# Kernel tuning notes

Measured on AMD Instinct MI355X. Metric: run time of the kernel, lower is better.

## Reference

```python
import jax, jax.numpy as jnp
import numpy as np

N = 10000      # nodes (docstring: dense mode intended for <=10k nodes)
D_IN = 64      # in_dim
D_OUT = 64     # out_dim


def setup_inputs() -> dict:
    key = jax.random.key(0)
    kH, kA1, kA2, kA3, kW1, kW2, kW3 = jax.random.split(key, 7)
    H = jax.random.normal(kH, (N, D_IN), dtype=jnp.float32)
    # Dense normalized adjacency per edge type (values in [0,1), as in A_norm)
    A_r1 = jax.random.uniform(kA1, (N, N), dtype=jnp.float32)
    A_r2 = jax.random.uniform(kA2, (N, N), dtype=jnp.float32)
    A_r3 = jax.random.uniform(kA3, (N, N), dtype=jnp.float32)
    # Xavier-uniform init for type-specific linear weights [out_dim, in_dim]
    limit = float(np.sqrt(6.0 / (D_IN + D_OUT)))
    W1 = jax.random.uniform(kW1, (D_OUT, D_IN), dtype=jnp.float32, minval=-limit, maxval=limit)
    W2 = jax.random.uniform(kW2, (D_OUT, D_IN), dtype=jnp.float32, minval=-limit, maxval=limit)
    W3 = jax.random.uniform(kW3, (D_OUT, D_IN), dtype=jnp.float32, minval=-limit, maxval=limit)
    bias = jnp.zeros((D_OUT,), dtype=jnp.float32)
    return {"H": H, "A_r1": A_r1, "A_r2": A_r2, "A_r3": A_r3,
            "W1": W1, "W2": W2, "W3": W3, "bias": bias}


def reference(H, A_r1, A_r2, A_r3, W1, W2, W3, bias):
    # h_v = sum_r W_r @ (sum_u A_r[v,u] * h_u) + b  (no activation in forward)
    out = bias  # broadcasts to [N, D_OUT]
    for A_r, W_r in ((A_r1, W1), (A_r2, W2), (A_r3, W3)):
        msg = A_r @ H                      # [N, D_IN] neighbor aggregation
        out = out + msg @ W_r.T            # [N, D_OUT] type-specific projection
    return out
```

## Files before the change

### kernel.cpp

```cpp
#include <hip/hip_runtime.h>

static constexpr int NN = 10000;
static constexpr int DD = 64;
static constexpr int KP = 10240;
static constexpr int BK = 128;
static constexpr int SPLITS = 4;
static constexpr int KC = KP / SPLITS;
static constexpr int ITERS = KC / BK;
static constexpr int BM = 64;

typedef __attribute__((ext_vector_type(4))) float f32x4;
typedef __attribute__((ext_vector_type(8))) short s16x8;

__device__ __forceinline__ unsigned short f2bf(float f) {
  unsigned u = __float_as_uint(f);
  return (unsigned short)((u + 0x7fffu + ((u >> 16) & 1u)) >> 16);
}

__device__ __forceinline__ void g2l16(const void* g, void* l) {
  __builtin_amdgcn_global_load_lds((const __attribute__((address_space(1))) unsigned int*)g,
                                   (__attribute__((address_space(3))) unsigned int*)l, 16, 0, 0);
}

__global__ void prep_kernel(const float* __restrict__ H,
                            const float* __restrict__ W1,
                            const float* __restrict__ W2,
                            const float* __restrict__ W3,
                            unsigned short* __restrict__ mt) {
  const int r = blockIdx.y;
  const float* W = (r == 0) ? W1 : (r == 1) ? W2 : W3;
  const int wave = threadIdx.x >> 6;
  const int lane = threadIdx.x & 63;
  f32x4 wr[16];
#pragma unroll
  for (int i = 0; i < 16; ++i) wr[i] = *(const f32x4*)&W[lane * 64 + i * 4];
  unsigned short* orow = mt + ((size_t)r * 64 + lane) * KP;
  const int kbase = blockIdx.x * 128 + wave * 32;
  for (int i = 0; i < 32; ++i) {
    const int k = kbase + i;
    if (k < NN) {
      float s = 0.f;
#pragma unroll
      for (int j = 0; j < 16; ++j) {
        f32x4 h = *(const f32x4*)&H[(size_t)k * 64 + j * 4];
        s += h[0] * wr[j][0] + h[1] * wr[j][1] + h[2] * wr[j][2] + h[3] * wr[j][3];
      }
      orow[k] = f2bf(s);
    } else {
      orow[k] = 0;
    }
  }
}

__global__ void init_out_kernel(const float* __restrict__ bias, float* __restrict__ out) {
  const int i = blockIdx.x * 256 + threadIdx.x;
  if (i < NN * DD) out[i] = bias[i & 63];
}

__global__ __launch_bounds__(256, 4) void gcn_main(const float* __restrict__ A1,
                                                   const float* __restrict__ A2,
                                                   const float* __restrict__ A3,
                                                   const unsigned short* __restrict__ mt,
                                                   float* __restrict__ out) {
  __shared__ __align__(1024) unsigned short mlds[2][64][128];

  const int r = blockIdx.z;
  const int s = blockIdx.y;
  const float* A = (r == 0) ? A1 : (r == 1) ? A2 : A3;
  const unsigned short* mtr = mt + (size_t)r * 64 * KP;

  const int wave = threadIdx.x >> 6;
  const int lane = threadIdx.x & 63;
  const int l15 = lane & 15;
  const int lhi = lane >> 4;
  const int seg = lane & 15;
  const int r16 = lane >> 4;
  const int v0 = blockIdx.x * BM;
  const int k0 = s * KC;

  int vA = v0 + wave * 16 + l15;
  if (vA > NN - 1) vA = NN - 1;
  const float* arow = A + (size_t)vA * NN;

  f32x4 acc[4] = {{0.f,0.f,0.f,0.f},{0.f,0.f,0.f,0.f},{0.f,0.f,0.f,0.f},{0.f,0.f,0.f,0.f}};
  f32x4 R0[4][2], R1[4][2];

  auto stageM = [&](int t, int buf) {
    const int kb = k0 + t * BK;
#pragma unroll
    for (int j = 0; j < 4; ++j) {
      const int row16 = 4 * j + r16;
      const int rowabs = wave * 16 + row16;
      const unsigned short* src = mtr + (size_t)rowabs * KP + kb + ((seg ^ row16) << 3);
      g2l16(src, &mlds[buf][wave * 16 + 4 * j][0]);
    }
  };

  auto issueA = [&](f32x4 (&a)[4][2], int kb) {
    if (kb + BK <= NN) {
      const float* p = arow + kb + lhi * 8;
      asm volatile(
        "global_load_dwordx4 %0, %8, off\n\t"
        "global_load_dwordx4 %1, %8, off offset:16\n\t"
        "global_load_dwordx4 %2, %8, off offset:128\n\t"
        "global_load_dwordx4 %3, %8, off offset:144\n\t"
        "global_load_dwordx4 %4, %8, off offset:256\n\t"
        "global_load_dwordx4 %5, %8, off offset:272\n\t"
        "global_load_dwordx4 %6, %8, off offset:384\n\t"
        "global_load_dwordx4 %7, %8, off offset:400"
        : "=&v"(a[0][0]), "=&v"(a[0][1]), "=&v"(a[1][0]), "=&v"(a[1][1]),
          "=&v"(a[2][0]), "=&v"(a[2][1]), "=&v"(a[3][0]), "=&v"(a[3][1])
        : "v"(p));
    } else {
      const int kf0 = kb + lhi * 8;
      const float* q0 = arow + ((kf0       < NN) ? kf0       : 0);
      const float* q1 = arow + ((kf0 + 4   < NN) ? kf0 + 4   : 0);
      const float* q2 = arow + ((kf0 + 32  < NN) ? kf0 + 32  : 0);
      const float* q3 = arow + ((kf0 + 36  < NN) ? kf0 + 36  : 0);
      const float* q4 = arow + ((kf0 + 64  < NN) ? kf0 + 64  : 0);
      const float* q5 = arow + ((kf0 + 68  < NN) ? kf0 + 68  : 0);
      const float* q6 = arow + ((kf0 + 96  < NN) ? kf0 + 96  : 0);
      const float* q7 = arow + ((kf0 + 100 < NN) ? kf0 + 100 : 0);
      asm volatile(
        "global_load_dwordx4 %0, %8, off\n\t"
        "global_load_dwordx4 %1, %9, off\n\t"
        "global_load_dwordx4 %2, %10, off\n\t"
        "global_load_dwordx4 %3, %11, off\n\t"
        "global_load_dwordx4 %4, %12, off\n\t"
        "global_load_dwordx4 %5, %13, off\n\t"
        "global_load_dwordx4 %6, %14, off\n\t"
        "global_load_dwordx4 %7, %15, off"
        : "=&v"(a[0][0]), "=&v"(a[0][1]), "=&v"(a[1][0]), "=&v"(a[1][1]),
          "=&v"(a[2][0]), "=&v"(a[2][1]), "=&v"(a[3][0]), "=&v"(a[3][1])
        : "v"(q0), "v"(q1), "v"(q2), "v"(q3), "v"(q4), "v"(q5), "v"(q6), "v"(q7));
    }
  };

  auto cvtA = [&](const f32x4& x, const f32x4& y) -> s16x8 {
    s16x8 v;
    v[0] = (short)f2bf(x[0]); v[1] = (short)f2bf(x[1]);
    v[2] = (short)f2bf(x[2]); v[3] = (short)f2bf(x[3]);
    v[4] = (short)f2bf(y[0]); v[5] = (short)f2bf(y[1]);
    v[6] = (short)f2bf(y[2]); v[7] = (short)f2bf(y[3]);
    return v;
  };

  auto body = [&](int t, f32x4 (&cur)[4][2], f32x4 (&nxt)[4][2]) {
    const int tn = (t + 1 < ITERS) ? t + 1 : ITERS - 1;
    issueA(nxt, k0 + tn * BK);
    stageM(tn, (t + 1) & 1);
    __builtin_amdgcn_sched_barrier(0);
    asm volatile("s_waitcnt vmcnt(12)");
    __builtin_amdgcn_sched_barrier(0);
    __builtin_amdgcn_s_barrier();
    const int kb = k0 + t * BK;
    const int buf = t & 1;
    if (kb + BK > NN) {
      const f32x4 z = {0.f, 0.f, 0.f, 0.f};
#pragma unroll
      for (int kk = 0; kk < 4; ++kk) {
        const int kf = kb + kk * 32 + lhi * 8;
        cur[kk][0] = (kf     >= NN) ? z : cur[kk][0];
        cur[kk][1] = (kf + 4 >= NN) ? z : cur[kk][1];
      }
    }
#pragma unroll
    for (int kk = 0; kk < 4; ++kk) {
      s16x8 a = cvtA(cur[kk][0], cur[kk][1]);
#pragma unroll
      for (int dt = 0; dt < 4; ++dt) {
        const int g = kk * 4 + lhi;
        s16x8 b = *(const s16x8*)&mlds[buf][dt * 16 + l15][((g ^ l15) & 15) * 8];
        acc[dt] = __builtin_amdgcn_mfma_f32_16x16x32_bf16(a, b, acc[dt], 0, 0, 0);
      }
    }
    __builtin_amdgcn_sched_barrier(0);
    __builtin_amdgcn_s_barrier();
  };

  issueA(R0, k0);
  stageM(0, 0);

  for (int t = 0; t < ITERS; t += 2) {
    body(t, R0, R1);
    body(t + 1, R1, R0);
  }

  asm volatile("s_waitcnt vmcnt(0)");

#pragma unroll
  for (int dt = 0; dt < 4; ++dt) {
    const int d = dt * 16 + l15;
#pragma unroll
    for (int i = 0; i < 4; ++i) {
      const int v = v0 + wave * 16 + lhi * 4 + i;
      if (v < NN) atomicAdd(&out[(size_t)v * DD + d], acc[dt][i]);
    }
  }
}

extern "C" void kernel_launch(void* const* d_in, const int* in_sizes, int n_in,
                              void* d_out, int out_size, void* d_ws, size_t ws_size,
                              hipStream_t stream) {
  const float* H    = (const float*)d_in[0];
  const float* A1   = (const float*)d_in[1];
  const float* A2   = (const float*)d_in[2];
  const float* A3   = (const float*)d_in[3];
  const float* W1   = (const float*)d_in[4];
  const float* W2   = (const float*)d_in[5];
  const float* W3   = (const float*)d_in[6];
  const float* bias = (const float*)d_in[7];
  float* out = (float*)d_out;
  unsigned short* mt = (unsigned short*)d_ws;

  prep_kernel<<<dim3(KP / 128, 3), 256, 0, stream>>>(H, W1, W2, W3, mt);
  init_out_kernel<<<dim3((NN * DD + 255) / 256), 256, 0, stream>>>(bias, out);
  gcn_main<<<dim3((NN + BM - 1) / BM, SPLITS, 3), 256, 0, stream>>>(A1, A2, A3, mt, out);
}
```

Baseline: 310.1 us.

## Stage whole M chunk in LDS once and raise K splits

Raises the K split count so each block handles only four 128-wide K tiles. The block's full 64x512 bf16 slice of the projected features is loaded into LDS once up front, replacing per-tile double-buffered staging and the two barriers per iteration. The A loads then run as a fixed, fully unrolled two-register-set pipeline gated by explicit vmcnt waits. The aim is to cut synchronisation and give more blocks to saturate HBM bandwidth on the dense adjacency stream. The costs are 64KB of LDS per block with lower occupancy (launch bounds 2), five times more atomicAdd traffic to the output, and dropping the explicit tail masking, which now relies on the zero-padded M.

```diff
diff --git a/kernel.cpp b/kernel.cpp
--- a/kernel.cpp
+++ b/kernel.cpp
@@ -4,7 +4,7 @@
 static constexpr int DD = 64;
 static constexpr int KP = 10240;
 static constexpr int BK = 128;
-static constexpr int SPLITS = 4;
+static constexpr int SPLITS = 20;
 static constexpr int KC = KP / SPLITS;
 static constexpr int ITERS = KC / BK;
 static constexpr int BM = 64;
@@ -57,12 +57,12 @@
   if (i < NN * DD) out[i] = bias[i & 63];
 }
 
-__global__ __launch_bounds__(256, 4) void gcn_main(const float* __restrict__ A1,
+__global__ __launch_bounds__(256, 2) void gcn_main(const float* __restrict__ A1,
                                                    const float* __restrict__ A2,
                                                    const float* __restrict__ A3,
                                                    const unsigned short* __restrict__ mt,
                                                    float* __restrict__ out) {
-  __shared__ __align__(1024) unsigned short mlds[2][64][128];
+  __shared__ __align__(1024) unsigned short mlds[64][512];
 
   const int r = blockIdx.z;
   const int s = blockIdx.y;
@@ -73,8 +73,6 @@
   const int lane = threadIdx.x & 63;
   const int l15 = lane & 15;
   const int lhi = lane >> 4;
-  const int seg = lane & 15;
-  const int r16 = lane >> 4;
   const int v0 = blockIdx.x * BM;
   const int k0 = s * KC;
 
@@ -83,20 +81,17 @@
   const float* arow = A + (size_t)vA * NN;
 
   f32x4 acc[4] = {{0.f,0.f,0.f,0.f},{0.f,0.f,0.f,0.f},{0.f,0.f,0.f,0.f},{0.f,0.f,0.f,0.f}};
-  f32x4 R0[4][2], R1[4][2];
-
-  auto stageM = [&](int t, int buf) {
-    const int kb = k0 + t * BK;
-#pragma unroll
-    for (int j = 0; j < 4; ++j) {
-      const int row16 = 4 * j + r16;
-      const int rowabs = wave * 16 + row16;
-      const unsigned short* src = mtr + (size_t)rowabs * KP + kb + ((seg ^ row16) << 3);
-      g2l16(src, &mlds[buf][wave * 16 + 4 * j][0]);
-    }
-  };
-
-  auto issueA = [&](f32x4 (&a)[4][2], int kb) {
+  f32x4 R0[8], R1[8];
+
+#pragma unroll
+  for (int j = 0; j < 16; ++j) {
+    const int d = wave * 16 + j;
+    const int gsrc = (lane & 48) | ((lane & 15) ^ (d & 15));
+    const unsigned short* src = mtr + (size_t)d * KP + k0 + gsrc * 8;
+    g2l16(src, &mlds[d][0]);
+  }
+
+  auto issueA = [&](f32x4 (&a)[8], int kb) {
     if (kb + BK <= NN) {
       const float* p = arow + kb + lhi * 8;
       asm volatile(
@@ -108,8 +103,8 @@
         "global_load_dwordx4 %5, %8, off offset:272\n\t"
         "global_load_dwordx4 %6, %8, off offset:384\n\t"
         "global_load_dwordx4 %7, %8, off offset:400"
-        : "=&v"(a[0][0]), "=&v"(a[0][1]), "=&v"(a[1][0]), "=&v"(a[1][1]),
-          "=&v"(a[2][0]), "=&v"(a[2][1]), "=&v"(a[3][0]), "=&v"(a[3][1])
+        : "=&v"(a[0]), "=&v"(a[1]), "=&v"(a[2]), "=&v"(a[3]),
+          "=&v"(a[4]), "=&v"(a[5]), "=&v"(a[6]), "=&v"(a[7])
         : "v"(p));
     } else {
       const int kf0 = kb + lhi * 8;
@@ -130,8 +125,8 @@
         "global_load_dwordx4 %5, %13, off\n\t"
         "global_load_dwordx4 %6, %14, off\n\t"
         "global_load_dwordx4 %7, %15, off"
-        : "=&v"(a[0][0]), "=&v"(a[0][1]), "=&v"(a[1][0]), "=&v"(a[1][1]),
-          "=&v"(a[2][0]), "=&v"(a[2][1]), "=&v"(a[3][0]), "=&v"(a[3][1])
+        : "=&v"(a[0]), "=&v"(a[1]), "=&v"(a[2]), "=&v"(a[3]),
+          "=&v"(a[4]), "=&v"(a[5]), "=&v"(a[6]), "=&v"(a[7])
         : "v"(q0), "v"(q1), "v"(q2), "v"(q3), "v"(q4), "v"(q5), "v"(q6), "v"(q7));
     }
   };
@@ -145,48 +140,47 @@
     return v;
   };
 
-  auto body = [&](int t, f32x4 (&cur)[4][2], f32x4 (&nxt)[4][2]) {
-    const int tn = (t + 1 < ITERS) ? t + 1 : ITERS - 1;
-    issueA(nxt, k0 + tn * BK);
-    stageM(tn, (t + 1) & 1);
-    __builtin_amdgcn_sched_barrier(0);
-    asm volatile("s_waitcnt vmcnt(12)");
-    __builtin_amdgcn_sched_barrier(0);
-    __builtin_amdgcn_s_barrier();
-    const int kb = k0 + t * BK;
-    const int buf = t & 1;
-    if (kb + BK > NN) {
-      const f32x4 z = {0.f, 0.f, 0.f, 0.f};
-#pragma unroll
-      for (int kk = 0; kk < 4; ++kk) {
-        const int kf = kb + kk * 32 + lhi * 8;
-        cur[kk][0] = (kf     >= NN) ? z : cur[kk][0];
-        cur[kk][1] = (kf + 4 >= NN) ? z : cur[kk][1];
+  auto mfmaTile = [&](f32x4 (&a)[8], int t) {
+#pragma unroll
+    for (int kk = 0; kk < 4; ++kk) {
+      s16x8 av = cvtA(a[2 * kk], a[2 * kk + 1]);
+#pragma unroll
+      for (int dt = 0; dt < 4; ++dt) {
+        const int slot = t * 16 + ((kk * 4 + lhi) ^ l15);
+        s16x8 b = *(const s16x8*)&mlds[dt * 16 + l15][slot * 8];
+        acc[dt] = __builtin_amdgcn_mfma_f32_16x16x32_bf16(av, b, acc[dt], 0, 0, 0);
       }
     }
-#pragma unroll
-    for (int kk = 0; kk < 4; ++kk) {
-      s16x8 a = cvtA(cur[kk][0], cur[kk][1]);
-#pragma unroll
-      for (int dt = 0; dt < 4; ++dt) {
-        const int g = kk * 4 + lhi;
-        s16x8 b = *(const s16x8*)&mlds[buf][dt * 16 + l15][((g ^ l15) & 15) * 8];
-        acc[dt] = __builtin_amdgcn_mfma_f32_16x16x32_bf16(a, b, acc[dt], 0, 0, 0);
-      }
-    }
-    __builtin_amdgcn_sched_barrier(0);
-    __builtin_amdgcn_s_barrier();
   };
 
   issueA(R0, k0);
-  stageM(0, 0);
-
-  for (int t = 0; t < ITERS; t += 2) {
-    body(t, R0, R1);
-    body(t + 1, R1, R0);
-  }
-
+  __builtin_amdgcn_sched_barrier(0);
+  issueA(R1, k0 + BK);
+  __builtin_amdgcn_sched_barrier(0);
+  asm volatile("s_waitcnt vmcnt(16)");
+  __builtin_amdgcn_sched_barrier(0);
+  __builtin_amdgcn_s_barrier();
+  __builtin_amdgcn_sched_barrier(0);
+
+  asm volatile("s_waitcnt vmcnt(8)");
+  __builtin_amdgcn_sched_barrier(0);
+  mfmaTile(R0, 0);
+  __builtin_amdgcn_sched_barrier(0);
+  issueA(R0, k0 + 2 * BK);
+  __builtin_amdgcn_sched_barrier(0);
+  asm volatile("s_waitcnt vmcnt(8)");
+  __builtin_amdgcn_sched_barrier(0);
+  mfmaTile(R1, 1);
+  __builtin_amdgcn_sched_barrier(0);
+  issueA(R1, k0 + 3 * BK);
+  __builtin_amdgcn_sched_barrier(0);
+  asm volatile("s_waitcnt vmcnt(8)");
+  __builtin_amdgcn_sched_barrier(0);
+  mfmaTile(R0, 2);
+  __builtin_amdgcn_sched_barrier(0);
   asm volatile("s_waitcnt vmcnt(0)");
+  __builtin_amdgcn_sched_barrier(0);
+  mfmaTile(R1, 3);
 
 #pragma unroll
   for (int dt = 0; dt < 4; ++dt) {
```

New measurement: 304.8 us. About the same (-1.7%).
